# Kernel optimization log

Hardware: AMD Instinct MI355X
Metric: run time of the kernel (lower is better)

The kernel has to match this reference:

```python
import jax, jax.numpy as jnp
import numpy as np

NB, SL, NH, EN, NE, HEADS = 8, 512, 512, 16, 64, 2
NEG = -1e9  # stand-in for -inf key_padding_mask fill (no row is fully masked)


def setup_inputs() -> dict:
    key = jax.random.key(0)
    ks = jax.random.split(key, 12)
    s = 0.02
    tokens_embed = jax.random.normal(ks[0], (NB, SL, NH), dtype=jnp.float32)
    events_embed = jax.random.normal(ks[1], (NE, NH), dtype=jnp.float32)
    entities = jax.random.uniform(ks[2], (NB, EN, SL)) < 0.3
    entities = entities.at[:, :, 0].set(True)  # guarantee >=1 attendable token per entity
    entity_masks = jnp.ones((NB, EN), dtype=bool)
    select_event = jnp.ones((NB, NE), dtype=bool)
    Wq = jax.random.normal(ks[3], (NH, NH), dtype=jnp.float32) * s
    Wk = jax.random.normal(ks[4], (NH, NH), dtype=jnp.float32) * s
    Wv = jax.random.normal(ks[5], (NH, NH), dtype=jnp.float32) * s
    bq = jax.random.normal(ks[6], (NH,), dtype=jnp.float32) * s
    bk = jax.random.normal(ks[7], (NH,), dtype=jnp.float32) * s
    bv = jax.random.normal(ks[8], (NH,), dtype=jnp.float32) * s
    Wo = jax.random.normal(ks[9], (NH, NH), dtype=jnp.float32) * s
    bo = jax.random.normal(ks[10], (NH,), dtype=jnp.float32) * s
    return dict(tokens_embed=tokens_embed, entities=entities, events_embed=events_embed,
                entity_num=EN, entity_masks=entity_masks, select_event=select_event,
                Wq=Wq, Wk=Wk, Wv=Wv, bq=bq, bk=bk, bv=bv, Wo=Wo, bo=bo)


def reference(tokens_embed, entities, events_embed, entity_num, entity_masks,
              select_event, Wq, Wk, Wv, bq, bk, bv, Wo, bo):
    nbatch, seq_len, nhid = tokens_embed.shape
    nevents = events_embed.shape[0]
    dh = nhid // HEADS
    scale = 1.0 / np.sqrt(dh).astype(np.float32)

    # which (batch, entity) slots are real entities -> flat indices (ragged select)
    entity_index = jnp.flatnonzero(entity_masks.reshape(-1))            # [N]
    # which (entity, event) pairs survive select_event & entity_masks
    pair_sel = (select_event[:, None, :] & entity_masks[:, :, None])    # [B, EN, NE]
    pair_sel = pair_sel.reshape(-1, nevents)[entity_index].reshape(-1)  # [N*NE]
    event_entity_index = jnp.flatnonzero(pair_sel)

    # key padding mask: True = ignore token (inverse of entity span mask)
    attn_mask = ~entities.reshape(-1, seq_len)[entity_index]            # [N, S]

    # gather per-entity token sequences (equivalent to repeat+index in torch code)
    batch_of = entity_index // entity_num
    toks = tokens_embed[batch_of]                                        # [N, S, nhid]

    # torch MultiheadAttention math: shared in-proj split into q/k/v, per-head SDPA
    q = (events_embed @ Wq.T + bq).reshape(nevents, HEADS, dh)           # shared across N
    k = (toks @ Wk.T + bk).reshape(-1, seq_len, HEADS, dh)               # [N, S, H, dh]
    v = (toks @ Wv.T + bv).reshape(-1, seq_len, HEADS, dh)

    scores = jnp.einsum('ehd,nshd->nhes', q, k) * scale                  # [N, H, NE, S]
    scores = jnp.where(attn_mask[:, None, None, :], NEG, scores)
    attn = jax.nn.softmax(scores, axis=-1)
    out = jnp.einsum('nhes,nshd->nehd', attn, v).reshape(-1, nevents, nhid)
    out = out @ Wo.T + bo                                                # [N, NE, nhid]

    return out.reshape(-1, nhid)[event_entity_index]
```

## Files before the change

kernel.cpp:

```cpp
#include <hip/hip_runtime.h>


#define NB 8
#define SL 512
#define NH 512
#define EN 16
#define NE 64
#define HEADS 2
#define DH 256
#define SCALE 0.0625f

typedef __attribute__((ext_vector_type(8))) short short8;
typedef __attribute__((ext_vector_type(4))) short short4v;
typedef __attribute__((ext_vector_type(4))) float f32x4;

#define MFMA16(a, b, c) __builtin_amdgcn_mfma_f32_16x16x32_bf16(a, b, c, 0, 0, 0)

__device__ __forceinline__ short f2b(float f) {
    unsigned u = __builtin_bit_cast(unsigned, f);
    u += 0x7fffu + ((u >> 16) & 1u);
    return (short)(u >> 16);
}
__device__ __forceinline__ float b2f(short s) {
    return __builtin_bit_cast(float, ((unsigned)(unsigned short)s) << 16);
}
__device__ __forceinline__ int swz8(int hw, int chunk) {
    return (hw & 7) * chunk + (hw >> 3);
}

__device__ __forceinline__ void gload16(const short* g, short* l) {
    __builtin_amdgcn_global_load_lds(
        (const __attribute__((address_space(1))) unsigned int*)g,
        (__attribute__((address_space(3))) unsigned int*)l, 16, 0, 0);
}

__device__ __forceinline__ void mm42(f32x4 (&acc)[4][2], const short8 (&a)[4], const short8 (&bb)[2]) {
#pragma unroll
    for (int i = 0; i < 4; ++i)
#pragma unroll
        for (int j = 0; j < 2; ++j) acc[i][j] = MFMA16(a[i], bb[j], acc[i][j]);
}
__device__ __forceinline__ void mm44(f32x4 (&acc)[4][4], const short8 (&a)[4], const short8 (&bb)[4]) {
#pragma unroll
    for (int i = 0; i < 4; ++i)
#pragma unroll
        for (int j = 0; j < 4; ++j) acc[i][j] = MFMA16(a[i], bb[j], acc[i][j]);
}

#define WS_TOKS 0u
#define WS_K (4u << 20)
#define WS_V (8u << 20)
#define WS_S (20u << 20)
#define WS_WK (22u << 20)
#define WS_WV (WS_WK + (512u << 10))
#define WS_WO (WS_WV + (512u << 10))
#define WS_WQ (WS_WO + (512u << 10))
#define WS_EV (WS_WQ + (512u << 10))
#define WS_Q (WS_EV + (64u << 10))
#define WS_FLAG (WS_Q + (64u << 10))
#define WS_VW (32u << 20)
#define WS_P (40u << 20)

#define CH_TOKS (NB * SL * NH / 4)
#define CH_W (NH * NH / 4)
#define CH_EV (NE * NH / 4)
#define CH_TOTAL (CH_TOKS + 4 * CH_W + CH_EV)

__global__ void prep_kernel(const float* __restrict__ toks, const float* __restrict__ Wk,
                            const float* __restrict__ Wv, const float* __restrict__ Wo,
                            const float* __restrict__ Wq, const float* __restrict__ ev,
                            const unsigned char* __restrict__ ents,
                            short* __restrict__ toks_bf, short* __restrict__ Wk_bf,
                            short* __restrict__ Wv_bf, short* __restrict__ Wo_bf,
                            short* __restrict__ Wq_bf, short* __restrict__ ev_bf,
                            int* __restrict__ flag) {
    __shared__ int red[256];
    int idx = blockIdx.x * 256 + threadIdx.x;
    if (idx < CH_TOTAL) {
        const float* src;
        short* dst;
        int off = idx;
        if (idx < CH_TOKS) { src = toks; dst = toks_bf; }
        else if (idx < CH_TOKS + CH_W) { src = Wk; dst = Wk_bf; off -= CH_TOKS; }
        else if (idx < CH_TOKS + 2 * CH_W) { src = Wv; dst = Wv_bf; off -= CH_TOKS + CH_W; }
        else if (idx < CH_TOKS + 3 * CH_W) { src = Wo; dst = Wo_bf; off -= CH_TOKS + 2 * CH_W; }
        else if (idx < CH_TOKS + 4 * CH_W) { src = Wq; dst = Wq_bf; off -= CH_TOKS + 3 * CH_W; }
        else { src = ev; dst = ev_bf; off -= CH_TOKS + 4 * CH_W; }
        f32x4 v = ((const f32x4*)src)[off];
        short4v o;
#pragma unroll
        for (int j = 0; j < 4; ++j) o[j] = f2b(v[j]);
        ((short4v*)dst)[off] = o;
    }
    if (blockIdx.x == gridDim.x - 1) {
        int tid = threadIdx.x;
        int cnt = 0;
        for (int j = 0; j < 16; ++j) {
            int off = tid * 16 + j;
            if ((off & 3) != 0 && ents[off] != 0) cnt++;
        }
        red[tid] = cnt;
        __syncthreads();
        for (int s = 128; s > 0; s >>= 1) {
            if (tid < s) red[tid] += red[tid + s];
            __syncthreads();
        }
        if (tid == 0) flag[0] = (red[0] == 0) ? 1 : 0;
    }
}

__device__ __forceinline__ void m97_core128(
    const short* __restrict__ Ag, int lda,
    const short* __restrict__ Bg, int ldb, int K,
    short* Alds, short* Blds, int wid, int lane, f32x4 (&acc)[4][4]) {
    int wm = wid >> 1, wn = wid & 1;
    int l15 = lane & 15;
    int rl = lane >> 3;
    int xb = (lane & 7) << 4;
    int kx = (xb ^ (rl << 4)) >> 1;

    const short* aG0 = Ag + (size_t)(wid * 8 + rl) * lda + kx;
    const short* bG0 = Bg + (size_t)(wid * 8 + rl) * ldb + kx;
    size_t aCs = (size_t)32 * lda;
    size_t bCs = (size_t)32 * ldb;

    auto stage = [&](int k0, int buf) {
        short* aL0 = Alds + buf * 8192 + wid * 512;
        short* bL0 = Blds + buf * 8192 + wid * 512;
#pragma unroll
        for (int c = 0; c < 4; ++c) {
            gload16(aG0 + c * aCs + k0, aL0 + c * 2048);
            gload16(bG0 + c * bCs + k0, bL0 + c * 2048);
        }
    };
    auto compute = [&](int buf) {
        const char* Ab = (const char*)(Alds + buf * 8192);
        const char* Bb = (const char*)(Blds + buf * 8192);
#pragma unroll
        for (int kk = 0; kk < 2; ++kk) {
            int x = kk * 64 + ((lane >> 4) << 4);
            short8 af[4], bf_[4];
#pragma unroll
            for (int i = 0; i < 4; ++i) {
                int row = wm * 64 + i * 16 + l15;
                af[i] = *(const short8*)(Ab + row * 128 + (x ^ ((row & 7) << 4)));
            }
#pragma unroll
            for (int j = 0; j < 4; ++j) {
                int row = wn * 64 + j * 16 + l15;
                bf_[j] = *(const short8*)(Bb + row * 128 + (x ^ ((row & 7) << 4)));
            }
            mm44(acc, af, bf_);
        }
    };

    int nsteps = K >> 6;
    stage(0, 0);
    stage(64, 1);
    asm volatile("s_waitcnt vmcnt(8)" ::: "memory");
    __builtin_amdgcn_sched_barrier(0);
    __builtin_amdgcn_s_barrier();

    int buf = 0;
    for (int s = 0; s < nsteps; ++s, buf ^= 1) {
        compute(buf);
        if (s + 1 < nsteps) {
            __builtin_amdgcn_s_barrier();
            if (s + 2 < nsteps) {
                stage((s + 2) * 64, buf);
                asm volatile("s_waitcnt vmcnt(8)" ::: "memory");
            } else {
                asm volatile("s_waitcnt vmcnt(0)" ::: "memory");
            }
            __builtin_amdgcn_sched_barrier(0);
            __builtin_amdgcn_s_barrier();
        }
    }
}

__device__ __forceinline__ void m97_core64(
    const short* __restrict__ Ag, int lda,
    const short* __restrict__ Bg, int ldb, int K,
    short* Alds, short* Blds, int wid, int lane, f32x4 (&acc)[4][2]) {
    int l15 = lane & 15;
    int rl = lane >> 3;
    int xb = (lane & 7) << 4;
    int kx = (xb ^ (rl << 4)) >> 1;

    const short* aG0 = Ag + (size_t)(wid * 8 + rl) * lda + kx;
    const short* bG0 = Bg + (size_t)(wid * 8 + rl) * ldb + kx;
    size_t aCs = (size_t)32 * lda;
    size_t bCs = (size_t)32 * ldb;

    auto stage = [&](int k0, int buf) {
        short* aL0 = Alds + buf * 4096 + wid * 512;
        short* bL0 = Blds + buf * 8192 + wid * 512;
        gload16(aG0 + k0, aL0);
        gload16(aG0 + aCs + k0, aL0 + 2048);
#pragma unroll
        for (int c = 0; c < 4; ++c)
            gload16(bG0 + c * bCs + k0, bL0 + c * 2048);
    };
    auto compute = [&](int buf) {
        const char* Ab = (const char*)(Alds + buf * 4096);
        const char* Bb = (const char*)(Blds + buf * 8192);
#pragma unroll
        for (int kk = 0; kk < 2; ++kk) {
            int x = kk * 64 + ((lane >> 4) << 4);
            short8 af[4], bf_[2];
#pragma unroll
            for (int i = 0; i < 4; ++i) {
                int row = i * 16 + l15;
                af[i] = *(const short8*)(Ab + row * 128 + (x ^ ((row & 7) << 4)));
            }
#pragma unroll
            for (int j = 0; j < 2; ++j) {
                int row = wid * 32 + j * 16 + l15;
                bf_[j] = *(const short8*)(Bb + row * 128 + (x ^ ((row & 7) << 4)));
            }
            mm42(acc, af, bf_);
        }
    };

    int nsteps = K >> 6;
    stage(0, 0);
    stage(64, 1);
    asm volatile("s_waitcnt vmcnt(6)" ::: "memory");
    __builtin_amdgcn_sched_barrier(0);
    __builtin_amdgcn_s_barrier();

    int buf = 0;
    for (int s = 0; s < nsteps; ++s, buf ^= 1) {
        compute(buf);
        if (s + 1 < nsteps) {
            __builtin_amdgcn_s_barrier();
            if (s + 2 < nsteps) {
                stage((s + 2) * 64, buf);
                asm volatile("s_waitcnt vmcnt(6)" ::: "memory");
            } else {
                asm volatile("s_waitcnt vmcnt(0)" ::: "memory");
            }
            __builtin_amdgcn_sched_barrier(0);
            __builtin_amdgcn_s_barrier();
        }
    }
}

__global__ void __launch_bounds__(256, 2)
projn(const short* __restrict__ toks_bf,
      const short* __restrict__ Wk_bf,
      const short* __restrict__ Wv_bf,
      const short* __restrict__ ev_bf,
      const short* __restrict__ Wq_bf,
      const float* __restrict__ bk, const float* __restrict__ bv,
      const float* __restrict__ bq,
      short* __restrict__ K_bf, short* __restrict__ V_bf,
      short* __restrict__ q_bf) {
    __shared__ short Alds[2 * 128 * 64];
    __shared__ short Blds[2 * 128 * 64];
    int t = blockIdx.x;
    int tid = threadIdx.x, lane = tid & 63, wid = tid >> 6;
    int l15 = lane & 15;
    int crow = (lane >> 4) * 4;

    if (t < 256) {
        int l = swz8(t, 32);
        int b = l >> 5, kind = (l >> 4) & 1, mt = (l >> 2) & 3, nt = l & 3;
        const short* Ag = toks_bf + (size_t)(b * SL + mt * 128) * NH;
        const short* Bg = (kind ? Wv_bf : Wk_bf) + (size_t)(nt * 128) * NH;
        const float* bias = kind ? bv : bk;
        short* dst = kind ? V_bf : K_bf;

        f32x4 acc[4][4];
#pragma unroll
        for (int i = 0; i < 4; ++i)
#pragma unroll
            for (int j = 0; j < 4; ++j) acc[i][j] = (f32x4)0.f;

        m97_core128(Ag, NH, Bg, NH, NH, Alds, Blds, wid, lane, acc);

        int wm = wid >> 1, wn = wid & 1;
#pragma unroll
        for (int i = 0; i < 4; ++i)
#pragma unroll
            for (int j = 0; j < 4; ++j) {
                int col = nt * 128 + wn * 64 + j * 16 + l15;
                float bval = bias[col];
                int row0 = b * SL + mt * 128 + wm * 64 + i * 16 + crow;
#pragma unroll
                for (int r = 0; r < 4; ++r)
                    dst[(size_t)(row0 + r) * NH + col] = f2b(acc[i][j][r] + bval);
            }
    } else {
        int tq = t - 256;
        const short* Ag = ev_bf;
        const short* Bg = Wq_bf + (size_t)(tq * 128) * NH;

        f32x4 acc[4][2];
#pragma unroll
        for (int i = 0; i < 4; ++i)
#pragma unroll
            for (int j = 0; j < 2; ++j) acc[i][j] = (f32x4)0.f;

        m97_core64(Ag, NH, Bg, NH, NH, Alds, Blds, wid, lane, acc);

#pragma unroll
        for (int i = 0; i < 4; ++i)
#pragma unroll
            for (int j = 0; j < 2; ++j) {
                int col = tq * 128 + wid * 32 + j * 16 + l15;
                float bval = bq[col];
#pragma unroll
                for (int r = 0; r < 4; ++r) {
                    int row = i * 16 + crow + r;
                    q_bf[(size_t)row * NH + col] = f2b((acc[i][j][r] + bval) * SCALE);
                }
            }
    }
}

__global__ void __launch_bounds__(256, 2)
vwtn_scores(const short* __restrict__ V_bf,
            const short* __restrict__ Wo_bf,
            const short* __restrict__ q_bf,
            const short* __restrict__ K_bf,
            short* __restrict__ VWt,
            short* __restrict__ S_bf) {
    __shared__ short Alds[2 * 128 * 64];
    __shared__ short Blds[2 * 128 * 64];
    int t = blockIdx.x;
    int tid = threadIdx.x, lane = tid & 63, wid = tid >> 6;
    int l15 = lane & 15;
    int crow = (lane >> 4) * 4;

    if (t < 256) {
        int l = swz8(t, 32);
        int bh = l >> 4, mt = (l >> 2) & 3, nt = l & 3;
        int b = bh >> 1, h = bh & 1;

        const short* Ag = Wo_bf + (size_t)(mt * 128) * NH + h * DH;
        const short* Bg = V_bf + (size_t)(b * SL + nt * 128) * NH + h * DH;

        f32x4 acc[4][4];
#pragma unroll
        for (int i = 0; i < 4; ++i)
#pragma unroll
            for (int j = 0; j < 4; ++j) acc[i][j] = (f32x4)0.f;

        m97_core128(Ag, NH, Bg, NH, DH, Alds, Blds, wid, lane, acc);

        int wm = wid >> 1, wn = wid & 1;
        short* dst = VWt + (size_t)b * NH * 1024 + h * 512;
#pragma unroll
        for (int i = 0; i < 4; ++i)
#pragma unroll
            for (int j = 0; j < 4; ++j) {
                int col = nt * 128 + wn * 64 + j * 16 + l15;
                int row0 = mt * 128 + wm * 64 + i * 16 + crow;
#pragma unroll
                for (int r = 0; r < 4; ++r)
                    dst[(size_t)(row0 + r) * 1024 + col] = f2b(acc[i][j][r]);
            }
    } else {
        int l = swz8(t - 256, 8);
        int b = l >> 3, h = (l >> 2) & 1, st = l & 3;

        const short* Ag = q_bf + h * DH;
        const short* Bg = K_bf + (size_t)(b * SL + st * 128) * NH + h * DH;

        f32x4 acc[4][2];
#pragma unroll
        for (int i = 0; i < 4; ++i)
#pragma unroll
            for (int j = 0; j < 2; ++j) acc[i][j] = (f32x4)0.f;

        m97_core64(Ag, NH, Bg, NH, DH, Alds, Blds, wid, lane, acc);

#pragma unroll
        for (int i = 0; i < 4; ++i)
#pragma unroll
            for (int j = 0; j < 2; ++j) {
                int col = st * 128 + wid * 32 + j * 16 + l15;
#pragma unroll
                for (int r = 0; r < 4; ++r) {
                    int row = i * 16 + crow + r;
                    S_bf[(((size_t)(b * HEADS + h)) * NE + row) * SL + col] = f2b(__expf(acc[i][j][r]));
                }
            }
    }
}

__global__ void __launch_bounds__(256, 4)
pnorm_kernel(const short* __restrict__ S_bf,
             const void* __restrict__ ents,
             const int* __restrict__ flag,
             short* __restrict__ P) {
    int l = swz8(blockIdx.x, 32);
    int b = l >> 5, ent = (l >> 1) & 15, eh = l & 1;
    int tid = threadIdx.x, lane = tid & 63, wid = tid >> 6;

    unsigned att8 = 0;
    {
        size_t mbase = ((size_t)b * EN + ent) * SL + lane * 8;
        if (flag[0]) {
            const int* p = (const int*)ents;
#pragma unroll
            for (int j = 0; j < 8; ++j)
                if (p[mbase + j]) att8 |= 1u << j;
        } else {
            const unsigned char* p = (const unsigned char*)ents;
#pragma unroll
            for (int j = 0; j < 8; ++j)
                if (p[mbase + j]) att8 |= 1u << j;
        }
    }

    for (int it = 0; it < 8; ++it) {
        int e = eh * 32 + wid * 8 + it;
        const short* s0p = S_bf + (((size_t)(b * HEADS + 0)) * NE + e) * SL + lane * 8;
        const short* s1p = S_bf + (((size_t)(b * HEADS + 1)) * NE + e) * SL + lane * 8;
        short8 v0 = *(const short8*)s0p;
        short8 v1 = *(const short8*)s1p;
        float f0[8], f1[8], sum0 = 0.f, sum1 = 0.f;
#pragma unroll
        for (int j = 0; j < 8; ++j) {
            f0[j] = (att8 >> j & 1) ? b2f(v0[j]) : 0.f;
            f1[j] = (att8 >> j & 1) ? b2f(v1[j]) : 0.f;
            sum0 += f0[j];
            sum1 += f1[j];
        }
#pragma unroll
        for (int off = 32; off; off >>= 1) {
            sum0 += __shfl_xor(sum0, off);
            sum1 += __shfl_xor(sum1, off);
        }
        float iv0 = 1.f / sum0, iv1 = 1.f / sum1;
        short8 o0, o1;
#pragma unroll
        for (int j = 0; j < 8; ++j) {
            o0[j] = f2b(f0[j] * iv0);
            o1[j] = f2b(f1[j] * iv1);
        }
        short* prow = P + ((size_t)(b * EN + ent) * NE + e) * 1024;
        *(short8*)(prow + lane * 8) = o0;
        *(short8*)(prow + 512 + lane * 8) = o1;
    }
}

__global__ void __launch_bounds__(256, 2)
outg(const short* __restrict__ P,
     const short* __restrict__ VWt,
     const float* __restrict__ bo,
     float* __restrict__ out) {
    __shared__ short Alds[2 * 128 * 64];
    __shared__ short Blds[2 * 128 * 64];
    int l = swz8(blockIdx.x, 32);
    int b = l >> 5, mt = (l >> 2) & 7, nt = l & 3;
    int tid = threadIdx.x, lane = tid & 63, wid = tid >> 6;
    int l15 = lane & 15;
    int crow = (lane >> 4) * 4;

    const short* Ag = P + ((size_t)b * 1024 + mt * 128) * 1024;
    const short* Bg = VWt + ((size_t)b * NH + nt * 128) * 1024;

    f32x4 acc[4][4];
#pragma unroll
    for (int i = 0; i < 4; ++i)
#pragma unroll
        for (int j = 0; j < 4; ++j) acc[i][j] = (f32x4)0.f;

    m97_core128(Ag, 1024, Bg, 1024, 1024, Alds, Blds, wid, lane, acc);

    int wm = wid >> 1, wn = wid & 1;
    int gr0 = b * 1024 + mt * 128 + wm * 64;
#pragma unroll
    for (int i = 0; i < 4; ++i)
#pragma unroll
        for (int j = 0; j < 4; ++j) {
            int col = nt * 128 + wn * 64 + j * 16 + l15;
            float bval = bo[col];
#pragma unroll
            for (int r = 0; r < 4; ++r) {
                int row = gr0 + i * 16 + crow + r;
                out[(size_t)row * NH + col] = acc[i][j][r] + bval;
            }
        }
}

extern "C" void kernel_launch(void* const* d_in, const int* in_sizes, int n_in,
                              void* d_out, int out_size, void* d_ws, size_t ws_size,
                              hipStream_t stream) {
    const float* toks = (const float*)d_in[0];
    const void* ents = d_in[1];
    const float* evs = (const float*)d_in[2];
    const float* Wq = (const float*)d_in[6];
    const float* Wk = (const float*)d_in[7];
    const float* Wv = (const float*)d_in[8];
    const float* bq = (const float*)d_in[9];
    const float* bk = (const float*)d_in[10];
    const float* bv = (const float*)d_in[11];
    const float* Wo = (const float*)d_in[12];
    const float* bo = (const float*)d_in[13];

    char* ws = (char*)d_ws;
    short* toks_bf = (short*)(ws + WS_TOKS);
    short* K_bf = (short*)(ws + WS_K);
    short* V_bf = (short*)(ws + WS_V);
    short* S_bf = (short*)(ws + WS_S);
    short* Wk_bf = (short*)(ws + WS_WK);
    short* Wv_bf = (short*)(ws + WS_WV);
    short* Wo_bf = (short*)(ws + WS_WO);
    short* Wq_bf = (short*)(ws + WS_WQ);
    short* ev_bf = (short*)(ws + WS_EV);
    short* q_bf = (short*)(ws + WS_Q);
    int* flag = (int*)(ws + WS_FLAG);
    short* VWt = (short*)(ws + WS_VW);
    short* P = (short*)(ws + WS_P);

    prep_kernel<<<CH_TOTAL / 256 + 1, 256, 0, stream>>>(
        toks, Wk, Wv, Wo, Wq, evs, (const unsigned char*)ents,
        toks_bf, Wk_bf, Wv_bf, Wo_bf, Wq_bf, ev_bf, flag);
    projn<<<260, 256, 0, stream>>>(toks_bf, Wk_bf, Wv_bf, ev_bf, Wq_bf,
                                   bk, bv, bq, K_bf, V_bf, q_bf);
    vwtn_scores<<<320, 256, 0, stream>>>(V_bf, Wo_bf, q_bf, K_bf, VWt, S_bf);
    pnorm_kernel<<<256, 256, 0, stream>>>(S_bf, ents, flag, P);
    outg<<<256, 256, 0, stream>>>(P, VWt, bo, (float*)d_out);
}
```

Baseline: 51.37 us.

## Fuse softmax normalization into output GEMM A-operand staging, drop materialized P

Instead of writing a normalized per-entity probability matrix P (16x larger than S) to global memory and reading it back in the output GEMM, a small kernel now computes only masked row sums and their inverses. The output GEMM loads the shared exp-scores S directly, applies the entity mask and inverse sum while writing into LDS, and stages VWt with async loads in a double-buffered pipeline. This removes the large P write/read traffic at the cost of extra ALU work and register pressure inside the GEMM loop.

Result: slower. 64.08 us (+24.7%).

```diff
diff --git a/kernel.cpp b/kernel.cpp
--- a/kernel.cpp
+++ b/kernel.cpp
@@ -59,7 +59,7 @@
 #define WS_Q (WS_EV + (64u << 10))
 #define WS_FLAG (WS_Q + (64u << 10))
 #define WS_VW (32u << 20)
-#define WS_P (40u << 20)
+#define WS_INV (40u << 20)
 
 #define CH_TOKS (NB * SL * NH / 4)
 #define CH_W (NH * NH / 4)
@@ -391,77 +391,65 @@
 }
 
 __global__ void __launch_bounds__(256, 4)
-pnorm_kernel(const short* __restrict__ S_bf,
-             const void* __restrict__ ents,
-             const int* __restrict__ flag,
-             short* __restrict__ P) {
+sums_kernel(const short* __restrict__ S_bf,
+            const void* __restrict__ ents,
+            const int* __restrict__ flag,
+            float* __restrict__ inv) {
+    __shared__ unsigned mask_lds[16];
     int l = swz8(blockIdx.x, 32);
-    int b = l >> 5, ent = (l >> 1) & 15, eh = l & 1;
-    int tid = threadIdx.x, lane = tid & 63, wid = tid >> 6;
-
-    unsigned att8 = 0;
-    {
-        size_t mbase = ((size_t)b * EN + ent) * SL + lane * 8;
+    int b = l >> 5, ent = (l >> 1) & 15, h = l & 1;
+    int tid = threadIdx.x;
+    if (tid < 16) {
+        size_t base = ((size_t)b * EN + ent) * SL + tid * 32;
+        unsigned m = 0;
         if (flag[0]) {
             const int* p = (const int*)ents;
-#pragma unroll
-            for (int j = 0; j < 8; ++j)
-                if (p[mbase + j]) att8 |= 1u << j;
+            for (int j = 0; j < 32; ++j)
+                if (p[base + j]) m |= 1u << j;
         } else {
             const unsigned char* p = (const unsigned char*)ents;
-#pragma unroll
-            for (int j = 0; j < 8; ++j)
-                if (p[mbase + j]) att8 |= 1u << j;
-        }
-    }
-
-    for (int it = 0; it < 8; ++it) {
-        int e = eh * 32 + wid * 8 + it;
-        const short* s0p = S_bf + (((size_t)(b * HEADS + 0)) * NE + e) * SL + lane * 8;
-        const short* s1p = S_bf + (((size_t)(b * HEADS + 1)) * NE + e) * SL + lane * 8;
-        short8 v0 = *(const short8*)s0p;
-        short8 v1 = *(const short8*)s1p;
-        float f0[8], f1[8], sum0 = 0.f, sum1 = 0.f;
-#pragma unroll
-        for (int j = 0; j < 8; ++j) {
-            f0[j] = (att8 >> j & 1) ? b2f(v0[j]) : 0.f;
-            f1[j] = (att8 >> j & 1) ? b2f(v1[j]) : 0.f;
-            sum0 += f0[j];
-            sum1 += f1[j];
-        }
-#pragma unroll
-        for (int off = 32; off; off >>= 1) {
-            sum0 += __shfl_xor(sum0, off);
-            sum1 += __shfl_xor(sum1, off);
-        }
-        float iv0 = 1.f / sum0, iv1 = 1.f / sum1;
-        short8 o0, o1;
-#pragma unroll
-        for (int j = 0; j < 8; ++j) {
-            o0[j] = f2b(f0[j] * iv0);
-            o1[j] = f2b(f1[j] * iv1);
-        }
-        short* prow = P + ((size_t)(b * EN + ent) * NE + e) * 1024;
-        *(short8*)(prow + lane * 8) = o0;
-        *(short8*)(prow + 512 + lane * 8) = o1;
-    }
+            for (int j = 0; j < 32; ++j)
+                if (p[base + j]) m |= 1u << j;
+        }
+        mask_lds[tid] = m;
+    }
+    __syncthreads();
+    int e = tid >> 2, part = tid & 3;
+    const short* sp = S_bf + (((size_t)(b * HEADS + h)) * NE + e) * SL + part * 128;
+    float s = 0.f;
+#pragma unroll
+    for (int c = 0; c < 16; ++c) {
+        short8 v = *(const short8*)(sp + c * 8);
+        int sidx = part * 128 + c * 8;
+        unsigned mb = mask_lds[sidx >> 5] >> (sidx & 31);
+#pragma unroll
+        for (int j = 0; j < 8; ++j)
+            if (mb >> j & 1) s += b2f(v[j]);
+    }
+    s += __shfl_xor(s, 1);
+    s += __shfl_xor(s, 2);
+    if (part == 0) inv[(((size_t)b * EN + ent) * HEADS + h) * NE + e] = 1.f / s;
 }
 
 __global__ void __launch_bounds__(256, 2)
-outg(const short* __restrict__ P,
-     const short* __restrict__ VWt,
-     const float* __restrict__ bo,
-     float* __restrict__ out) {
-    __shared__ short Alds[2 * 128 * 64];
-    __shared__ short Blds[2 * 128 * 64];
+outgf(const short* __restrict__ S_bf,
+      const short* __restrict__ VWt,
+      const void* __restrict__ ents,
+      const int* __restrict__ flag,
+      const float* __restrict__ inv,
+      const float* __restrict__ bo,
+      float* __restrict__ out) {
+    __shared__ short Ald[2][128 * 64];
+    __shared__ short Bld[2][128 * 64];
+    __shared__ unsigned mask_lds[2][16];
+    __shared__ float inv_lds[2][2][64];
+
     int l = swz8(blockIdx.x, 32);
     int b = l >> 5, mt = (l >> 2) & 7, nt = l & 3;
     int tid = threadIdx.x, lane = tid & 63, wid = tid >> 6;
-    int l15 = lane & 15;
-    int crow = (lane >> 4) * 4;
-
-    const short* Ag = P + ((size_t)b * 1024 + mt * 128) * 1024;
-    const short* Bg = VWt + ((size_t)b * NH + nt * 128) * 1024;
+    int l15 = lane & 15, crow = (lane >> 4) * 4;
+    int wm = wid >> 1, wn = wid & 1;
+    int ent0 = mt * 2;
 
     f32x4 acc[4][4];
 #pragma unroll
@@ -469,9 +457,123 @@
 #pragma unroll
         for (int j = 0; j < 4; ++j) acc[i][j] = (f32x4)0.f;
 
-    m97_core128(Ag, 1024, Bg, 1024, 1024, Alds, Blds, wid, lane, acc);
-
-    int wm = wid >> 1, wn = wid & 1;
+    if (tid < 32) {
+        int ei = tid >> 4, w = tid & 15;
+        size_t base = ((size_t)b * EN + ent0 + ei) * SL + w * 32;
+        unsigned m = 0;
+        if (flag[0]) {
+            const int* p = (const int*)ents;
+            for (int j = 0; j < 32; ++j)
+                if (p[base + j]) m |= 1u << j;
+        } else {
+            const unsigned char* p = (const unsigned char*)ents;
+            for (int j = 0; j < 32; ++j)
+                if (p[base + j]) m |= 1u << j;
+        }
+        mask_lds[ei][w] = m;
+    }
+    {
+        int ei = tid >> 7, hh = (tid >> 6) & 1, ee = tid & 63;
+        inv_lds[ei][hh][ee] = inv[(((size_t)b * EN + ent0 + ei) * HEADS + hh) * NE + ee];
+    }
+    __syncthreads();
+
+    int rl = lane >> 3;
+    int kx = (((lane & 7) << 4) ^ (rl << 4)) >> 1;
+    const short* bG0 = VWt + ((size_t)b * NH + nt * 128 + wid * 8 + rl) * 1024 + kx;
+    size_t bCs = (size_t)32 * 1024;
+    auto stageB = [&](int k0, int buf) {
+        short* bL0 = &Bld[buf][wid * 512];
+#pragma unroll
+        for (int c = 0; c < 4; ++c)
+            gload16(bG0 + c * bCs + k0, bL0 + c * 2048);
+    };
+
+    int ae = tid >> 2, aseg = (tid & 3) << 4;
+    struct BL { short8 r0, r1; };
+    auto bload = [&](int kk) -> BL {
+        int h = kk >> 9, s0 = kk & 511;
+        const short* sp = S_bf + (((size_t)(b * HEADS + h)) * NE + ae) * SL + s0 + aseg;
+        BL r;
+        r.r0 = *(const short8*)sp;
+        r.r1 = *(const short8*)(sp + 8);
+        return r;
+    };
+    auto bwrite = [&](BL bl, int kk, int buf) {
+        int h = kk >> 9, s0 = kk & 511;
+        int sbit = (s0 + aseg) & 31;
+        unsigned mword = (unsigned)(s0 + aseg) >> 5;
+#pragma unroll
+        for (int ei = 0; ei < 2; ++ei) {
+            float iv = inv_lds[ei][h][ae];
+            unsigned mbits = mask_lds[ei][mword] >> sbit;
+            int row = ei * 64 + ae;
+            short8 o0, o1;
+#pragma unroll
+            for (int j = 0; j < 8; ++j)
+                o0[j] = (mbits >> j & 1) ? f2b(b2f(bl.r0[j]) * iv) : (short)0;
+#pragma unroll
+            for (int j = 0; j < 8; ++j)
+                o1[j] = (mbits >> (8 + j) & 1) ? f2b(b2f(bl.r1[j]) * iv) : (short)0;
+            short* base = &Ald[buf][row * 64];
+            int g0 = aseg >> 3;
+            *(short8*)&base[((g0 ^ (row & 7)) << 3)] = o0;
+            *(short8*)&base[(((g0 + 1) ^ (row & 7)) << 3)] = o1;
+        }
+    };
+
+    auto compute = [&](int buf) {
+        const char* Ab = (const char*)&Ald[buf][0];
+        const char* Bb = (const char*)&Bld[buf][0];
+#pragma unroll
+        for (int kk = 0; kk < 2; ++kk) {
+            int x = kk * 64 + ((lane >> 4) << 4);
+            short8 af[4], bf_[4];
+#pragma unroll
+            for (int i = 0; i < 4; ++i) {
+                int row = wm * 64 + i * 16 + l15;
+                af[i] = *(const short8*)(Ab + row * 128 + (x ^ ((row & 7) << 4)));
+            }
+#pragma unroll
+            for (int j = 0; j < 4; ++j) {
+                int row = wn * 64 + j * 16 + l15;
+                bf_[j] = *(const short8*)(Bb + row * 128 + (x ^ ((row & 7) << 4)));
+            }
+            mm44(acc, af, bf_);
+        }
+    };
+
+    {
+        BL t0 = bload(0);
+        bwrite(t0, 0, 0);
+        stageB(0, 0);
+        BL t1 = bload(64);
+        bwrite(t1, 64, 1);
+        stageB(64, 1);
+        asm volatile("s_waitcnt vmcnt(0) lgkmcnt(0)" ::: "memory");
+        __builtin_amdgcn_sched_barrier(0);
+        __builtin_amdgcn_s_barrier();
+    }
+
+    int buf = 0;
+    BL pend2;
+    for (int s = 0; s < 16; ++s, buf ^= 1) {
+        if (s + 2 < 16) pend2 = bload((s + 2) * 64);
+        compute(buf);
+        if (s < 15) {
+            __builtin_amdgcn_s_barrier();
+            if (s + 2 < 16) {
+                stageB((s + 2) * 64, buf);
+                bwrite(pend2, (s + 2) * 64, buf);
+                asm volatile("s_waitcnt vmcnt(4) lgkmcnt(0)" ::: "memory");
+            } else {
+                asm volatile("s_waitcnt vmcnt(0) lgkmcnt(0)" ::: "memory");
+            }
+            __builtin_amdgcn_sched_barrier(0);
+            __builtin_amdgcn_s_barrier();
+        }
+    }
+
     int gr0 = b * 1024 + mt * 128 + wm * 64;
 #pragma unroll
     for (int i = 0; i < 4; ++i)
@@ -515,7 +617,7 @@
     short* q_bf = (short*)(ws + WS_Q);
     int* flag = (int*)(ws + WS_FLAG);
     short* VWt = (short*)(ws + WS_VW);
-    short* P = (short*)(ws + WS_P);
+    float* inv = (float*)(ws + WS_INV);
 
     prep_kernel<<<CH_TOTAL / 256 + 1, 256, 0, stream>>>(
         toks, Wk, Wv, Wo, Wq, evs, (const unsigned char*)ents,
@@ -523,6 +625,6 @@
     projn<<<260, 256, 0, stream>>>(toks_bf, Wk_bf, Wv_bf, ev_bf, Wq_bf,
                                    bk, bv, bq, K_bf, V_bf, q_bf);
     vwtn_scores<<<320, 256, 0, stream>>>(V_bf, Wo_bf, q_bf, K_bf, VWt, S_bf);
-    pnorm_kernel<<<256, 256, 0, stream>>>(S_bf, ents, flag, P);
-    outg<<<256, 256, 0, stream>>>(P, VWt, bo, (float*)d_out);
-}
+    sums_kernel<<<256, 256, 0, stream>>>(S_bf, ents, flag, inv);
+    outgf<<<256, 256, 0, stream>>>(S_bf, VWt, ents, flag, inv, bo, (float*)d_out);
+}
```
